# Optimization experiments

Hardware: AMD Instinct MI355X
Metric: run time of the kernel (lower is better)

Reference implementation:

```python
import jax, jax.numpy as jnp
import numpy as np

B, S, D, H = 2, 2048, 512, 8
HID = 512
DH = HID // H  # 64


def setup_inputs() -> dict:
    key = jax.random.key(0)
    ks = jax.random.split(key, 11)
    sc = 0.02
    return {
        "q": jax.random.normal(ks[0], (B, S, D), jnp.float32),
        "k": jax.random.normal(ks[1], (B, S, D), jnp.float32),
        "v": jax.random.normal(ks[2], (B, S, D), jnp.float32),
        "Wq": jax.random.normal(ks[3], (D, HID), jnp.float32) * sc,
        "bq": jnp.zeros((HID,), jnp.float32),
        "Wk": jax.random.normal(ks[4], (D, HID), jnp.float32) * sc,
        "bk": jnp.zeros((HID,), jnp.float32),
        "Wv": jax.random.normal(ks[5], (D, HID), jnp.float32) * sc,
        "bv": jnp.zeros((HID,), jnp.float32),
        "Wo": jax.random.normal(ks[6], (HID, D), jnp.float32) * sc,
        "bo": jnp.zeros((D,), jnp.float32),
    }


def reference(q, k, v, Wq, bq, Wk, bk, Wv, bv, Wo, bo):
    # Linear projections: [B,S,D] -> [B,S,HID]
    qp = q @ Wq + bq
    kp = k @ Wk + bk
    vp = v @ Wv + bv
    # Faithful to torch .view(B, -1, S, head_dim): raw reshape, NOT a
    # [B,S,H,d] transpose. Head i reads a contiguous block of the buffer.
    qh = qp.reshape(B, H, S, DH)
    kh = kp.reshape(B, H, S, DH)
    vh = vp.reshape(B, H, S, DH)
    # scores [B,H,S,S]; NOTE: original divides by sqrt(d) AFTER softmax.
    scores = jnp.einsum("bhsd,bhtd->bhst", qh, kh)
    attn = jax.nn.softmax(scores, axis=-1) / np.sqrt(DH).astype(np.float32)
    ctx = jnp.einsum("bhst,bhtd->bhsd", attn, vh)
    # torch.cat over heads along last dim -> [B,S,H*d] with head blocks
    concat = jnp.transpose(ctx, (0, 2, 1, 3)).reshape(B, S, HID)
    return concat @ Wo + bo
```

## Files before the change

kernel.cpp:

```cpp
#include <hip/hip_runtime.h>
#include <hip/hip_bf16.h>

typedef __bf16 bf16_t;
typedef __bf16 bf16x8 __attribute__((ext_vector_type(8)));
typedef float f32x4 __attribute__((ext_vector_type(4)));

static_assert(sizeof(bf16x8) == 16, "bf16x8 must be 16B");

#define BB 2
#define SS 2048
#define DD 512
#define HH 8
#define DH 64

__global__ void cast_qkv(const float* __restrict__ q, const float* __restrict__ k,
                         const float* __restrict__ v, bf16_t* __restrict__ dst, int n) {
  const float* src = (blockIdx.z == 0) ? q : (blockIdx.z == 1) ? k : v;
  bf16_t* out = dst + (size_t)blockIdx.z * n;
  int i = (blockIdx.x * 256 + threadIdx.x) * 8;
  if (i >= n) return;
  const float4* s4 = (const float4*)(src + i);
  float4 a = s4[0], b = s4[1];
  bf16x8 o;
  o[0] = (bf16_t)a.x; o[1] = (bf16_t)a.y; o[2] = (bf16_t)a.z; o[3] = (bf16_t)a.w;
  o[4] = (bf16_t)b.x; o[5] = (bf16_t)b.y; o[6] = (bf16_t)b.z; o[7] = (bf16_t)b.w;
  *(bf16x8*)(out + i) = o;
}

__global__ void transpose_w(const float* __restrict__ w0, const float* __restrict__ w1,
                            const float* __restrict__ w2, const float* __restrict__ w3,
                            bf16_t* __restrict__ wt) {
  __shared__ float tile[32][33];
  const float* W = (blockIdx.z == 0) ? w0 : (blockIdx.z == 1) ? w1 : (blockIdx.z == 2) ? w2 : w3;
  bf16_t* out = wt + (size_t)blockIdx.z * 512 * 512;
  int tx = threadIdx.x, ty = threadIdx.y;
  int nb = blockIdx.x * 32, kb = blockIdx.y * 32;
#pragma unroll
  for (int i = 0; i < 4; i++)
    tile[ty + i * 8][tx] = W[(size_t)(kb + ty + i * 8) * 512 + nb + tx];
  __syncthreads();
#pragma unroll
  for (int i = 0; i < 4; i++)
    out[(size_t)(nb + ty + i * 8) * 512 + kb + tx] = (bf16_t)tile[tx][ty + i * 8];
}

template <typename OutT>
__global__ __launch_bounds__(256) void gemm_bt(
    const bf16_t* __restrict__ Abase, const bf16_t* __restrict__ Btbase,
    const float* __restrict__ bias0, const float* __restrict__ bias1,
    const float* __restrict__ bias2, OutT* __restrict__ Cbase,
    int M, int N, int K, long Az, long Bz, long Cz) {
  const bf16_t* A  = Abase + (size_t)blockIdx.z * Az;
  const bf16_t* Bt = Btbase + (size_t)blockIdx.z * Bz;
  const float* bias = (blockIdx.z == 0) ? bias0 : (blockIdx.z == 1) ? bias1 : bias2;
  OutT* C = Cbase + (size_t)blockIdx.z * Cz;

  __shared__ bf16_t As[2][128 * 64];
  __shared__ bf16_t Bs[2][128 * 64];

  const int tid = threadIdx.x, w = tid >> 6, l = tid & 63;
  const int bm = blockIdx.y, bn = blockIdx.x;
  const int wm = (w >> 1) * 64, wn = (w & 1) * 64;
  const int lr = l & 15, lg = l >> 4;

  f32x4 acc[4][4] = {};

  auto stage = [&](int buf, int kt) {
#pragma unroll
    for (int j = 0; j < 4; j++) {
      int lin = (j * 4 + w) * 64 + l;
      int row = lin >> 3, cc = lin & 7;
      const bf16_t* g = A + (size_t)(bm * 128 + row) * K + kt * 64 + cc * 8;
      __builtin_amdgcn_global_load_lds(
          (const __attribute__((address_space(1))) void*)g,
          (__attribute__((address_space(3))) void*)(&As[buf][(j * 4 + w) * 512]), 16, 0, 0);
    }
#pragma unroll
    for (int j = 0; j < 4; j++) {
      int lin = (j * 4 + w) * 64 + l;
      int row = lin >> 3, cc = lin & 7;
      const bf16_t* g = Bt + (size_t)(bn * 128 + row) * K + kt * 64 + cc * 8;
      __builtin_amdgcn_global_load_lds(
          (const __attribute__((address_space(1))) void*)g,
          (__attribute__((address_space(3))) void*)(&Bs[buf][(j * 4 + w) * 512]), 16, 0, 0);
    }
  };

  stage(0, 0);
  const int KT = K >> 6;
  for (int kt = 0; kt < KT; kt++) {
    __syncthreads();
    if (kt + 1 < KT) stage((kt + 1) & 1, kt + 1);
    const bf16_t* as = As[kt & 1];
    const bf16_t* bs = Bs[kt & 1];
#pragma unroll
    for (int kc = 0; kc < 2; kc++) {
      bf16x8 a[4], b[4];
#pragma unroll
      for (int i = 0; i < 4; i++)
        a[i] = *(const bf16x8*)(as + (wm + i * 16 + lr) * 64 + kc * 32 + lg * 8);
#pragma unroll
      for (int i = 0; i < 4; i++)
        b[i] = *(const bf16x8*)(bs + (wn + i * 16 + lr) * 64 + kc * 32 + lg * 8);
#pragma unroll
      for (int i = 0; i < 4; i++)
#pragma unroll
        for (int j = 0; j < 4; j++)
          acc[i][j] = __builtin_amdgcn_mfma_f32_16x16x32_bf16(a[i], b[j], acc[i][j], 0, 0, 0);
    }
  }

  const int row0 = bm * 128 + wm, col0 = bn * 128 + wn;
#pragma unroll
  for (int j = 0; j < 4; j++) {
    int col = col0 + j * 16 + lr;
    float bv = bias[col];
#pragma unroll
    for (int i = 0; i < 4; i++) {
      int row = row0 + i * 16 + lg * 4;
#pragma unroll
      for (int r = 0; r < 4; r++) {
        float vv = acc[i][j][r] + bv;
        C[(size_t)(row + r) * N + col] = (OutT)vv;
      }
    }
  }
}

__global__ __launch_bounds__(256) void attn_flash(const bf16_t* __restrict__ qp,
                                                  const bf16_t* __restrict__ kp,
                                                  const bf16_t* __restrict__ vp,
                                                  bf16_t* __restrict__ ctx) {
  const int qt = blockIdx.x, bh = blockIdx.y;
  const int tid = threadIdx.x, w = tid >> 6, l = tid & 63;
  const int lr = l & 15, lg = l >> 4;
  const size_t hb = (size_t)bh * (SS * DH);
  const bf16_t* Q = qp + hb;
  const bf16_t* Kh = kp + hb;
  const bf16_t* Vh = vp + hb;

  __shared__ bf16_t Ks[2][64][72];
  __shared__ bf16_t Vt[2][64][72];
  __shared__ bf16_t Ps[4][16][72];

  const int qr0 = qt * 64 + w * 16;

  bf16x8 aq[2];
#pragma unroll
  for (int kc = 0; kc < 2; kc++)
    aq[kc] = *(const bf16x8*)(Q + (size_t)(qr0 + lr) * DH + kc * 32 + lg * 8);

  f32x4 o[4] = {};
  float m_r[4], l_r[4];
#pragma unroll
  for (int r = 0; r < 4; r++) { m_r[r] = -1e30f; l_r[r] = 0.f; }

  const int c0 = tid, c1 = 256 + tid;
  const int kr0 = c0 >> 3, kq0 = c0 & 7;
  const int kr1 = c1 >> 3, kq1 = c1 & 7;
  const int vk0 = c0 & 63, vd0 = (c0 >> 6) & 7;
  const int vk1 = c1 & 63, vd1 = (c1 >> 6) & 7;

  bf16x8 kreg0, kreg1, vreg0, vreg1;
  auto load_g = [&](int it) {
    const size_t kv0 = (size_t)it * 64;
    kreg0 = *(const bf16x8*)(Kh + (kv0 + kr0) * DH + kq0 * 8);
    kreg1 = *(const bf16x8*)(Kh + (kv0 + kr1) * DH + kq1 * 8);
    vreg0 = *(const bf16x8*)(Vh + (kv0 + vk0) * DH + vd0 * 8);
    vreg1 = *(const bf16x8*)(Vh + (kv0 + vk1) * DH + vd1 * 8);
  };
  auto write_lds = [&](int buf) {
    *(bf16x8*)(&Ks[buf][kr0][kq0 * 8]) = kreg0;
    *(bf16x8*)(&Ks[buf][kr1][kq1 * 8]) = kreg1;
#pragma unroll
    for (int j = 0; j < 8; j++) Vt[buf][vd0 * 8 + j][vk0] = vreg0[j];
#pragma unroll
    for (int j = 0; j < 8; j++) Vt[buf][vd1 * 8 + j][vk1] = vreg1[j];
  };

  load_g(0);
  write_lds(0);

  for (int it = 0; it < 32; it++) {
    const int buf = it & 1;
    __syncthreads();
    if (it + 1 < 32) load_g(it + 1);

    f32x4 s[4] = {};
    __builtin_amdgcn_s_setprio(1);
#pragma unroll
    for (int kc = 0; kc < 2; kc++) {
#pragma unroll
      for (int n = 0; n < 4; n++) {
        bf16x8 bk = *(const bf16x8*)(&Ks[buf][n * 16 + lr][kc * 32 + lg * 8]);
        s[n] = __builtin_amdgcn_mfma_f32_16x16x32_bf16(aq[kc], bk, s[n], 0, 0, 0);
      }
    }
    __builtin_amdgcn_s_setprio(0);

    float p[4][4];
#pragma unroll
    for (int r = 0; r < 4; r++) {
      float tmax = fmaxf(fmaxf(s[0][r], s[1][r]), fmaxf(s[2][r], s[3][r]));
#pragma unroll
      for (int msk = 1; msk < 16; msk <<= 1) tmax = fmaxf(tmax, __shfl_xor(tmax, msk));
      float mnew = fmaxf(m_r[r], tmax);
      float scale = __expf(m_r[r] - mnew);
      float rs = 0.f;
#pragma unroll
      for (int n = 0; n < 4; n++) { p[n][r] = __expf(s[n][r] - mnew); rs += p[n][r]; }
#pragma unroll
      for (int msk = 1; msk < 16; msk <<= 1) rs += __shfl_xor(rs, msk);
      l_r[r] = l_r[r] * scale + rs;
      m_r[r] = mnew;
#pragma unroll
      for (int n = 0; n < 4; n++) o[n][r] *= scale;
    }

#pragma unroll
    for (int n = 0; n < 4; n++)
#pragma unroll
      for (int r = 0; r < 4; r++)
        Ps[w][lg * 4 + r][n * 16 + lr] = (bf16_t)p[n][r];

    __builtin_amdgcn_s_setprio(1);
#pragma unroll
    for (int kc = 0; kc < 2; kc++) {
      bf16x8 pa = *(const bf16x8*)(&Ps[w][lr][kc * 32 + lg * 8]);
#pragma unroll
      for (int n = 0; n < 4; n++) {
        bf16x8 bv = *(const bf16x8*)(&Vt[buf][n * 16 + lr][kc * 32 + lg * 8]);
        o[n] = __builtin_amdgcn_mfma_f32_16x16x32_bf16(pa, bv, o[n], 0, 0, 0);
      }
    }
    __builtin_amdgcn_s_setprio(0);

    if (it + 1 < 32) write_lds(buf ^ 1);
  }

  const int b = bh >> 3, h = bh & 7;
#pragma unroll
  for (int r = 0; r < 4; r++) {
    float inv = 1.0f / (l_r[r] * 8.0f);
    int t = qr0 + lg * 4 + r;
    size_t rowbase = ((size_t)b * SS + t) * 512 + h * 64;
#pragma unroll
    for (int n = 0; n < 4; n++)
      ctx[rowbase + n * 16 + lr] = (bf16_t)(o[n][r] * inv);
  }
}

extern "C" void kernel_launch(void* const* d_in, const int* in_sizes, int n_in,
                              void* d_out, int out_size, void* d_ws, size_t ws_size,
                              hipStream_t stream) {
  const float* q  = (const float*)d_in[0];
  const float* k  = (const float*)d_in[1];
  const float* v  = (const float*)d_in[2];
  const float* Wq = (const float*)d_in[3];
  const float* bq = (const float*)d_in[4];
  const float* Wk = (const float*)d_in[5];
  const float* bk = (const float*)d_in[6];
  const float* Wv = (const float*)d_in[7];
  const float* bv = (const float*)d_in[8];
  const float* Wo = (const float*)d_in[9];
  const float* bo = (const float*)d_in[10];

  const size_t NQKV = (size_t)4096 * 512;
  const size_t NW = (size_t)512 * 512;

  bf16_t* ws  = (bf16_t*)d_ws;
  bf16_t* qkvb = ws;
  bf16_t* wt   = qkvb + 3 * NQKV;
  bf16_t* proj = wt + 4 * NW;
  bf16_t* ctx  = proj + 3 * NQKV;

  cast_qkv<<<dim3(1024, 1, 3), 256, 0, stream>>>(q, k, v, qkvb, (int)NQKV);
  transpose_w<<<dim3(16, 16, 4), dim3(32, 8), 0, stream>>>(Wq, Wk, Wv, Wo, wt);
  gemm_bt<bf16_t><<<dim3(4, 32, 3), 256, 0, stream>>>(
      qkvb, wt, bq, bk, bv, proj, 4096, 512, 512, (long)NQKV, (long)NW, (long)NQKV);
  attn_flash<<<dim3(32, 16), 256, 0, stream>>>(proj, proj + NQKV, proj + 2 * NQKV, ctx);
  gemm_bt<float><<<dim3(4, 32, 1), 256, 0, stream>>>(
      ctx, wt + 3 * NW, bo, bo, bo, (float*)d_out, 4096, 512, 512, 0, 0, 0);
}
```

Measured before the change: 110.6 us.

## Transpose QK^T MFMA to keep P in registers and feed PV directly

The QK^T MFMA operands are swapped so each lane holds a full column of scores for one query row. This turns the softmax row reductions into two cross-group shuffles instead of four-step butterflies per row. The probabilities are then fed straight into 16x16x16 bf16 MFMAs as the B operand, so the LDS round trip through the Ps buffer is dropped. The output is stored as vectorized bf16x4 writes. The cost is twice as many, smaller MFMA instructions for the PV product and 4-element V reads from LDS.

```diff
diff --git a/kernel.cpp b/kernel.cpp
--- a/kernel.cpp
+++ b/kernel.cpp
@@ -3,9 +3,17 @@
 
 typedef __bf16 bf16_t;
 typedef __bf16 bf16x8 __attribute__((ext_vector_type(8)));
+typedef __bf16 bf16x4 __attribute__((ext_vector_type(4)));
+typedef short short4v __attribute__((ext_vector_type(4)));
 typedef float f32x4 __attribute__((ext_vector_type(4)));
 
 static_assert(sizeof(bf16x8) == 16, "bf16x8 must be 16B");
+
+#if __has_builtin(__builtin_amdgcn_mfma_f32_16x16x16bf16_1k)
+#define HAS_MFMA16 1
+#else
+#define HAS_MFMA16 0
+#endif
 
 #define BB 2
 #define SS 2048
@@ -141,7 +149,9 @@
 
   __shared__ bf16_t Ks[2][64][72];
   __shared__ bf16_t Vt[2][64][72];
-  __shared__ bf16_t Ps[4][16][72];
+#if !HAS_MFMA16
+  __shared__ bf16_t Pq[4][16][72];
+#endif
 
   const int qr0 = qt * 64 + w * 16;
 
@@ -151,9 +161,7 @@
     aq[kc] = *(const bf16x8*)(Q + (size_t)(qr0 + lr) * DH + kc * 32 + lg * 8);
 
   f32x4 o[4] = {};
-  float m_r[4], l_r[4];
-#pragma unroll
-  for (int r = 0; r < 4; r++) { m_r[r] = -1e30f; l_r[r] = 0.f; }
+  float m_run = -1e30f, l_run = 0.f;
 
   const int c0 = tid, c1 = 256 + tid;
   const int kr0 = c0 >> 3, kq0 = c0 & 7;
@@ -193,40 +201,74 @@
 #pragma unroll
       for (int n = 0; n < 4; n++) {
         bf16x8 bk = *(const bf16x8*)(&Ks[buf][n * 16 + lr][kc * 32 + lg * 8]);
-        s[n] = __builtin_amdgcn_mfma_f32_16x16x32_bf16(aq[kc], bk, s[n], 0, 0, 0);
+        s[n] = __builtin_amdgcn_mfma_f32_16x16x32_bf16(bk, aq[kc], s[n], 0, 0, 0);
       }
     }
     __builtin_amdgcn_s_setprio(0);
 
-    float p[4][4];
+    float pmax = -1e30f;
+#pragma unroll
+    for (int n = 0; n < 4; n++)
+#pragma unroll
+      for (int r = 0; r < 4; r++) pmax = fmaxf(pmax, s[n][r]);
+    pmax = fmaxf(pmax, __shfl_xor(pmax, 16));
+    pmax = fmaxf(pmax, __shfl_xor(pmax, 32));
+    float mnew = fmaxf(m_run, pmax);
+    float scale = __expf(m_run - mnew);
+    m_run = mnew;
+    float rs = 0.f;
+#pragma unroll
+    for (int n = 0; n < 4; n++)
+#pragma unroll
+      for (int r = 0; r < 4; r++) {
+        float e = __expf(s[n][r] - mnew);
+        s[n][r] = e;
+        rs += e;
+      }
+    rs += __shfl_xor(rs, 16);
+    rs += __shfl_xor(rs, 32);
+    l_run = l_run * scale + rs;
+
+#if HAS_MFMA16
+#pragma unroll
+    for (int n = 0; n < 4; n++)
+#pragma unroll
+      for (int r = 0; r < 4; r++) o[n][r] *= scale;
+    short4v pb[4];
+#pragma unroll
+    for (int n = 0; n < 4; n++) {
+      bf16x4 t;
+#pragma unroll
+      for (int r = 0; r < 4; r++) t[r] = (bf16_t)s[n][r];
+      pb[n] = __builtin_bit_cast(short4v, t);
+    }
+    __builtin_amdgcn_s_setprio(1);
+#pragma unroll
+    for (int n = 0; n < 4; n++) {
+#pragma unroll
+      for (int c2 = 0; c2 < 4; c2++) {
+        bf16x4 bvh = *(const bf16x4*)(&Vt[buf][n * 16 + lr][c2 * 16 + lg * 4]);
+        o[n] = __builtin_amdgcn_mfma_f32_16x16x16bf16_1k(
+            __builtin_bit_cast(short4v, bvh), pb[c2], o[n], 0, 0, 0);
+      }
+    }
+    __builtin_amdgcn_s_setprio(0);
+#else
 #pragma unroll
     for (int r = 0; r < 4; r++) {
-      float tmax = fmaxf(fmaxf(s[0][r], s[1][r]), fmaxf(s[2][r], s[3][r]));
-#pragma unroll
-      for (int msk = 1; msk < 16; msk <<= 1) tmax = fmaxf(tmax, __shfl_xor(tmax, msk));
-      float mnew = fmaxf(m_r[r], tmax);
-      float scale = __expf(m_r[r] - mnew);
-      float rs = 0.f;
-#pragma unroll
-      for (int n = 0; n < 4; n++) { p[n][r] = __expf(s[n][r] - mnew); rs += p[n][r]; }
-#pragma unroll
-      for (int msk = 1; msk < 16; msk <<= 1) rs += __shfl_xor(rs, msk);
-      l_r[r] = l_r[r] * scale + rs;
-      m_r[r] = mnew;
-#pragma unroll
-      for (int n = 0; n < 4; n++) o[n][r] *= scale;
-    }
-
+      float sc = __shfl(scale, lg * 4 + r);
+#pragma unroll
+      for (int n = 0; n < 4; n++) o[n][r] *= sc;
+    }
 #pragma unroll
     for (int n = 0; n < 4; n++)
 #pragma unroll
       for (int r = 0; r < 4; r++)
-        Ps[w][lg * 4 + r][n * 16 + lr] = (bf16_t)p[n][r];
-
+        Pq[w][lr][n * 16 + lg * 4 + r] = (bf16_t)s[n][r];
     __builtin_amdgcn_s_setprio(1);
 #pragma unroll
     for (int kc = 0; kc < 2; kc++) {
-      bf16x8 pa = *(const bf16x8*)(&Ps[w][lr][kc * 32 + lg * 8]);
+      bf16x8 pa = *(const bf16x8*)(&Pq[w][lr][kc * 32 + lg * 8]);
 #pragma unroll
       for (int n = 0; n < 4; n++) {
         bf16x8 bv = *(const bf16x8*)(&Vt[buf][n * 16 + lr][kc * 32 + lg * 8]);
@@ -234,20 +276,37 @@
       }
     }
     __builtin_amdgcn_s_setprio(0);
+#endif
 
     if (it + 1 < 32) write_lds(buf ^ 1);
   }
 
   const int b = bh >> 3, h = bh & 7;
+#if HAS_MFMA16
+  {
+    float inv = 1.0f / (l_run * 8.0f);
+    int t = qr0 + lr;
+    size_t rowbase = ((size_t)b * SS + t) * 512 + h * 64;
+#pragma unroll
+    for (int n = 0; n < 4; n++) {
+      bf16x4 ov;
+#pragma unroll
+      for (int r = 0; r < 4; r++) ov[r] = (bf16_t)(o[n][r] * inv);
+      *(bf16x4*)(&ctx[rowbase + n * 16 + lg * 4]) = ov;
+    }
+  }
+#else
 #pragma unroll
   for (int r = 0; r < 4; r++) {
-    float inv = 1.0f / (l_r[r] * 8.0f);
+    float li = __shfl(l_run, lg * 4 + r);
+    float inv = 1.0f / (li * 8.0f);
     int t = qr0 + lg * 4 + r;
     size_t rowbase = ((size_t)b * SS + t) * 512 + h * 64;
 #pragma unroll
     for (int n = 0; n < 4; n++)
       ctx[rowbase + n * 16 + lr] = (bf16_t)(o[n][r] * inv);
   }
+#endif
 }
 
 extern "C" void kernel_launch(void* const* d_in, const int* in_sizes, int n_in,
```

Measured after the change: 91.40 us. 17.3% less time.
